# Performance work log

Measured on AMD Instinct MI355X. Metric: run time of the kernel, lower is better.

The kernel has to match this reference:

```python
import jax, jax.numpy as jnp
import numpy as np

K = 1024
D = 512
DECAY = 0.99


def setup_inputs() -> dict:
    key = jax.random.key(0)
    k1, k2, k3 = jax.random.split(key, 3)
    z_e_x = jax.random.normal(k1, (64, 256, D), dtype=jnp.float32)
    codebook = jax.random.normal(k2, (K, D), dtype=jnp.float32)
    ema_count = jnp.ones((K,), dtype=jnp.float32)
    ema_w = jax.random.normal(k3, (K, D), dtype=jnp.float32)
    return {"z_e_x": z_e_x, "codebook": codebook,
            "ema_count": ema_count, "ema_w": ema_w}


def reference(z_e_x, codebook, ema_count, ema_w):
    # --- vector quantization: nearest codebook entry (squared L2) ---
    flat = z_e_x.reshape(-1, D)                       # [N, D]
    cb_sqr = jnp.sum(codebook ** 2, axis=1)           # [K]
    in_sqr = jnp.sum(flat ** 2, axis=1, keepdims=True)  # [N, 1]
    distances = (cb_sqr[None, :] + in_sqr) - 2.0 * (flat @ codebook.T)  # [N, K]
    indices = jnp.argmin(distances, axis=1)           # [N] int

    # straight-through codes from current codebook
    z_q_x = codebook[indices].reshape(z_e_x.shape)

    # --- EMA codebook update (training branch) ---
    counts = jnp.zeros((K,), dtype=flat.dtype).at[indices].add(1.0)       # sum of one-hots
    new_ema_count = DECAY * ema_count + (1.0 - DECAY) * counts
    dw = jnp.zeros((K, D), dtype=flat.dtype).at[indices].add(flat)        # one_hot.T @ flat
    new_ema_w = DECAY * ema_w + (1.0 - DECAY) * dw
    new_embedding = new_ema_w / new_ema_count[:, None]

    # codes from the updated codebook
    z_q_x_bar = new_embedding[indices].reshape(z_e_x.shape)

    return (z_q_x, z_q_x_bar, new_embedding, new_ema_count, new_ema_w)
```

## Files before the change

### kernel.cpp

```cpp
#include <hip/hip_runtime.h>

typedef _Float16 half8  __attribute__((ext_vector_type(8)));
typedef float    f32x4  __attribute__((ext_vector_type(4)));

constexpr int K_CODES = 1024;
constexpr int D_DIM   = 512;
constexpr float DECAY = 0.99f;
constexpr float OMD   = 0.01f;
constexpr float LO_SCALE = 2048.0f;
constexpr float INV_LO   = 1.0f / 2048.0f;

constexpr int BM = 128;
constexpr int BN = 128;
constexpr int BK = 32;
constexpr int NPART = K_CODES / BN;
constexpr int CHUNK = 32;

__global__ __launch_bounds__(256) void zero_kernel(float4* __restrict__ p, int n4) {
    int i = blockIdx.x * 256 + threadIdx.x;
    if (i < n4) p[i] = make_float4(0.f, 0.f, 0.f, 0.f);
}

__global__ __launch_bounds__(64)
void prep_kernel(const float* __restrict__ cb, float* __restrict__ cbsqr,
                 float* __restrict__ counts,
                 _Float16* __restrict__ bh, _Float16* __restrict__ bl) {
    int k = blockIdx.x;
    int lane = threadIdx.x;
    size_t base = (size_t)k * D_DIM + lane * 8;
    f32x4 v0 = *reinterpret_cast<const f32x4*>(&cb[base]);
    f32x4 v1 = *reinterpret_cast<const f32x4*>(&cb[base + 4]);
    half8 h, l;
    float s = 0.f;
    #pragma unroll
    for (int j = 0; j < 4; ++j) {
        s += v0[j] * v0[j];
        _Float16 hh = (_Float16)v0[j];
        h[j] = hh;
        l[j] = (_Float16)((v0[j] - (float)hh) * LO_SCALE);
    }
    #pragma unroll
    for (int j = 0; j < 4; ++j) {
        s += v1[j] * v1[j];
        _Float16 hh = (_Float16)v1[j];
        h[4 + j] = hh;
        l[4 + j] = (_Float16)((v1[j] - (float)hh) * LO_SCALE);
    }
    *reinterpret_cast<half8*>(&bh[base]) = h;
    *reinterpret_cast<half8*>(&bl[base]) = l;
    #pragma unroll
    for (int off = 32; off > 0; off >>= 1) s += __shfl_down(s, off);
    if (lane == 0) { cbsqr[k] = s; counts[k] = 0.f; }
}

__global__ __launch_bounds__(256)
void splitA_kernel(const float* __restrict__ A,
                   _Float16* __restrict__ ah, _Float16* __restrict__ al) {
    size_t i8 = ((size_t)blockIdx.x * 256 + threadIdx.x) * 8;
    f32x4 v0 = *reinterpret_cast<const f32x4*>(&A[i8]);
    f32x4 v1 = *reinterpret_cast<const f32x4*>(&A[i8 + 4]);
    half8 h, l;
    #pragma unroll
    for (int j = 0; j < 4; ++j) {
        _Float16 hh = (_Float16)v0[j];
        h[j] = hh;
        l[j] = (_Float16)((v0[j] - (float)hh) * LO_SCALE);
    }
    #pragma unroll
    for (int j = 0; j < 4; ++j) {
        _Float16 hh = (_Float16)v1[j];
        h[4 + j] = hh;
        l[4 + j] = (_Float16)((v1[j] - (float)hh) * LO_SCALE);
    }
    *reinterpret_cast<half8*>(&ah[i8]) = h;
    *reinterpret_cast<half8*>(&al[i8]) = l;
}

__global__ __launch_bounds__(256, 2)
void argmin_mfma(const _Float16* __restrict__ Ah,
                 const _Float16* __restrict__ Al,
                 const _Float16* __restrict__ Bh,
                 const _Float16* __restrict__ Bl,
                 const float* __restrict__ cbsqr,
                 float* __restrict__ pval,
                 int*   __restrict__ pidx) {
    __shared__ _Float16 Ahs[BM * BK];
    __shared__ _Float16 Als[BM * BK];
    __shared__ _Float16 Bhs[BN * BK];
    __shared__ _Float16 Bls[BN * BK];
    __shared__ float    sv[2][BM];
    __shared__ int      si[2][BM];

    const int tid  = threadIdx.x;
    const int lane = tid & 63;
    const int wid  = tid >> 6;
    const int wr = wid >> 1, wc = wid & 1;
    const int lq = lane >> 4;
    const int lr = lane & 15;

    const int row0  = blockIdx.x * BM;
    const int cbase = blockIdx.y * BN;

    f32x4 acc_h[4][4], acc_c[4][4];
    #pragma unroll
    for (int m = 0; m < 4; ++m)
        #pragma unroll
        for (int n = 0; n < 4; ++n) {
            acc_h[m][n] = f32x4{0.f, 0.f, 0.f, 0.f};
            acc_c[m][n] = f32x4{0.f, 0.f, 0.f, 0.f};
        }

    for (int d0 = 0; d0 < D_DIM; d0 += BK) {
        #pragma unroll
        for (int it = 0; it < 2; ++it) {
            int p = it * 4096 + wid * 1024 + lane * 16;
            int row  = p >> 6;
            int cpos = (p >> 4) & 3;
            int sc   = cpos ^ ((row ^ (row >> 2)) & 3);
            size_t aoff = (size_t)(row0 + row) * D_DIM + d0 + sc * 8;
            size_t boff = (size_t)(cbase + row) * D_DIM + d0 + sc * 8;
            int dst = it * 2048 + wid * 512;
            __builtin_amdgcn_global_load_lds(
                (const __attribute__((address_space(1))) void*)(Ah + aoff),
                (__attribute__((address_space(3))) void*)(Ahs + dst), 16, 0, 0);
            __builtin_amdgcn_global_load_lds(
                (const __attribute__((address_space(1))) void*)(Al + aoff),
                (__attribute__((address_space(3))) void*)(Als + dst), 16, 0, 0);
            __builtin_amdgcn_global_load_lds(
                (const __attribute__((address_space(1))) void*)(Bh + boff),
                (__attribute__((address_space(3))) void*)(Bhs + dst), 16, 0, 0);
            __builtin_amdgcn_global_load_lds(
                (const __attribute__((address_space(1))) void*)(Bl + boff),
                (__attribute__((address_space(3))) void*)(Bls + dst), 16, 0, 0);
        }
        __syncthreads();

        half8 bh[4], bl[4];
        #pragma unroll
        for (int n = 0; n < 4; ++n) {
            int rB  = wc * 64 + n * 16 + lr;
            int pos = lq ^ ((rB ^ (rB >> 2)) & 3);
            bh[n] = *reinterpret_cast<const half8*>(&Bhs[rB * 32 + pos * 8]);
            bl[n] = *reinterpret_cast<const half8*>(&Bls[rB * 32 + pos * 8]);
        }
        #pragma unroll
        for (int m = 0; m < 4; ++m) {
            int rA  = wr * 64 + m * 16 + lr;
            int pos = lq ^ ((rA ^ (rA >> 2)) & 3);
            half8 ah = *reinterpret_cast<const half8*>(&Ahs[rA * 32 + pos * 8]);
            half8 al = *reinterpret_cast<const half8*>(&Als[rA * 32 + pos * 8]);
            #pragma unroll
            for (int n = 0; n < 4; ++n) {
                acc_h[m][n] = __builtin_amdgcn_mfma_f32_16x16x32_f16(ah, bh[n], acc_h[m][n], 0, 0, 0);
                acc_c[m][n] = __builtin_amdgcn_mfma_f32_16x16x32_f16(ah, bl[n], acc_c[m][n], 0, 0, 0);
                acc_c[m][n] = __builtin_amdgcn_mfma_f32_16x16x32_f16(al, bh[n], acc_c[m][n], 0, 0, 0);
            }
        }
        __syncthreads();
    }

    float cs[4];
    #pragma unroll
    for (int n = 0; n < 4; ++n) cs[n] = cbsqr[cbase + wc * 64 + n * 16 + lr];

    #pragma unroll
    for (int m = 0; m < 4; ++m) {
        #pragma unroll
        for (int q = 0; q < 4; ++q) {
            float bv = 3.4e38f;
            int   bi = 0;
            #pragma unroll
            for (int n = 0; n < 4; ++n) {
                float d = cs[n] - 2.0f * acc_h[m][n][q] - (2.0f * INV_LO) * acc_c[m][n][q];
                int   c = cbase + wc * 64 + n * 16 + lr;
                if (d < bv) { bv = d; bi = c; }
            }
            #pragma unroll
            for (int off = 1; off < 16; off <<= 1) {
                float v2 = __shfl_xor(bv, off);
                int   i2 = __shfl_xor(bi, off);
                if (v2 < bv || (v2 == bv && i2 < bi)) { bv = v2; bi = i2; }
            }
            if (lr == 0) {
                int prow = wr * 64 + m * 16 + lq * 4 + q;
                sv[wc][prow] = bv;
                si[wc][prow] = bi;
            }
        }
    }
    __syncthreads();
    if (tid < BM) {
        float v0 = sv[0][tid], v1 = sv[1][tid];
        int   i0 = si[0][tid], i1 = si[1][tid];
        float bv = (v1 < v0) ? v1 : v0;
        int   bi = (v1 < v0) ? i1 : i0;
        pval[(size_t)(row0 + tid) * NPART + blockIdx.y] = bv;
        pidx[(size_t)(row0 + tid) * NPART + blockIdx.y] = bi;
    }
}

__global__ __launch_bounds__(256)
void combine_kernel(const float* __restrict__ pval, const int* __restrict__ pidx,
                    int* __restrict__ indices, float* __restrict__ counts, int N) {
    int r = blockIdx.x * 256 + threadIdx.x;
    if (r >= N) return;
    float bv = pval[(size_t)r * NPART];
    int   bi = pidx[(size_t)r * NPART];
    #pragma unroll
    for (int p = 1; p < NPART; ++p) {
        float v = pval[(size_t)r * NPART + p];
        int  ii = pidx[(size_t)r * NPART + p];
        if (v < bv) { bv = v; bi = ii; }
    }
    indices[r] = bi;
    atomicAdd(&counts[bi], 1.0f);
}

__global__ __launch_bounds__(256)
void scan_kernel(const float* __restrict__ counts,
                 int* __restrict__ offs, int* __restrict__ cursor) {
    __shared__ int part[256];
    int t = threadIdx.x;
    int c[4], s = 0;
    #pragma unroll
    for (int j = 0; j < 4; ++j) { c[j] = (int)counts[t * 4 + j]; s += c[j]; }
    part[t] = s;
    __syncthreads();
    for (int off = 1; off < 256; off <<= 1) {
        int v   = part[t];
        int add = (t >= off) ? part[t - off] : 0;
        __syncthreads();
        part[t] = v + add;
        __syncthreads();
    }
    int run = part[t] - s;
    #pragma unroll
    for (int j = 0; j < 4; ++j) {
        offs[t * 4 + j]   = run;
        cursor[t * 4 + j] = run;
        run += c[j];
    }
    if (t == 255) offs[K_CODES] = part[255];
}

__global__ __launch_bounds__(256)
void scatter_kernel(const int* __restrict__ indices, int* __restrict__ cursor,
                    int* __restrict__ packed, int N) {
    int r = blockIdx.x * 256 + threadIdx.x;
    if (r >= N) return;
    int k = indices[r];
    int pos = atomicAdd(&cursor[k], 1);
    packed[pos] = (k << 16) | r;
}

__global__ __launch_bounds__(128)
void chunksum_kernel(const float* __restrict__ flat, const int* __restrict__ packed,
                     float* __restrict__ dw, int N) {
    __shared__ int ent[CHUNK + 1];
    const int t = threadIdx.x;
    const int base = blockIdx.x * CHUNK;
    const int cnt = min(CHUNK, N - base);
    if (t < cnt) ent[t] = packed[base + t];
    if (t == cnt) ent[t] = -1;
    __syncthreads();

    f32x4 acc = {0.f, 0.f, 0.f, 0.f};
    for (int i0 = 0; i0 < cnt; i0 += 8) {
        const int m = min(8, cnt - i0);
        f32x4 v[8];
        #pragma unroll
        for (int j = 0; j < 8; ++j) {
            if (j < m) {
                int r = ent[i0 + j] & 0xFFFF;
                v[j] = *reinterpret_cast<const f32x4*>(&flat[(size_t)r * D_DIM + t * 4]);
            }
        }
        #pragma unroll
        for (int j = 0; j < 8; ++j) {
            if (j < m) {
                acc[0] += v[j][0]; acc[1] += v[j][1];
                acc[2] += v[j][2]; acc[3] += v[j][3];
                int k = ent[i0 + j] >> 16;
                if ((ent[i0 + j + 1] >> 16) != k) {
                    float* p = &dw[(size_t)k * D_DIM + t * 4];
                    atomicAdd(p + 0, acc[0]);
                    atomicAdd(p + 1, acc[1]);
                    atomicAdd(p + 2, acc[2]);
                    atomicAdd(p + 3, acc[3]);
                    acc = f32x4{0.f, 0.f, 0.f, 0.f};
                }
            }
        }
    }
}

__global__ __launch_bounds__(256)
void finalize_kernel(const float* __restrict__ ema_count, const float* __restrict__ ema_w,
                     const float* __restrict__ counts, const float* __restrict__ dw,
                     float* __restrict__ new_emb, float* __restrict__ new_count,
                     float* __restrict__ new_ema_w) {
    int gid = blockIdx.x * 256 + threadIdx.x;
    int k = gid >> 7;
    int d = (gid & 127) * 4;
    float nc = DECAY * ema_count[k] + OMD * counts[k];
    size_t off = (size_t)k * D_DIM + d;
    float4 w  = *reinterpret_cast<const float4*>(&ema_w[off]);
    float4 dv = *reinterpret_cast<const float4*>(&dw[off]);
    float4 nw;
    nw.x = DECAY * w.x + OMD * dv.x;
    nw.y = DECAY * w.y + OMD * dv.y;
    nw.z = DECAY * w.z + OMD * dv.z;
    nw.w = DECAY * w.w + OMD * dv.w;
    *reinterpret_cast<float4*>(&new_ema_w[off]) = nw;
    float inv = 1.0f / nc;
    float4 ne;
    ne.x = nw.x * inv; ne.y = nw.y * inv; ne.z = nw.z * inv; ne.w = nw.w * inv;
    *reinterpret_cast<float4*>(&new_emb[off]) = ne;
    if ((gid & 127) == 0) new_count[k] = nc;
}

__global__ __launch_bounds__(256)
void gather_kernel(const float* __restrict__ codebook, const float* __restrict__ new_emb,
                   const int* __restrict__ indices,
                   float* __restrict__ zq, float* __restrict__ zqb) {
    int gid = blockIdx.x * 256 + threadIdx.x;
    int r = gid >> 7;
    int d = (gid & 127) * 4;
    int k = indices[r];
    size_t src = (size_t)k * D_DIM + d;
    size_t dst = (size_t)r * D_DIM + d;
    *reinterpret_cast<float4*>(&zq[dst])  = *reinterpret_cast<const float4*>(&codebook[src]);
    *reinterpret_cast<float4*>(&zqb[dst]) = *reinterpret_cast<const float4*>(&new_emb[src]);
}

extern "C" void kernel_launch(void* const* d_in, const int* in_sizes, int n_in,
                              void* d_out, int out_size, void* d_ws, size_t ws_size,
                              hipStream_t stream) {
    const float* z_e_x     = (const float*)d_in[0];
    const float* codebook  = (const float*)d_in[1];
    const float* ema_count = (const float*)d_in[2];
    const float* ema_w     = (const float*)d_in[3];

    const int N = in_sizes[0] / D_DIM;

    float* out = (float*)d_out;
    float* z_q_x     = out;
    float* z_q_x_bar = z_q_x + (size_t)N * D_DIM;
    float* new_emb   = z_q_x_bar + (size_t)N * D_DIM;
    float* new_count = new_emb + (size_t)K_CODES * D_DIM;
    float* new_ema_w = new_count + K_CODES;

    _Float16* Ahs = (_Float16*)z_q_x_bar;
    _Float16* Als = Ahs + (size_t)N * D_DIM;

    char* ws = (char*)d_ws;
    int*   indices = (int*)ws;
    float* cbsqr   = (float*)(ws + (size_t)N * 4);
    float* pval    = cbsqr + K_CODES;
    int*   pidx    = (int*)(pval + (size_t)N * NPART);
    float* counts  = (float*)(pidx + (size_t)N * NPART);
    _Float16* bh   = (_Float16*)(counts + K_CODES);
    _Float16* bl   = bh + (size_t)K_CODES * D_DIM;
    float* dw      = (float*)bh;
    int*   offs    = (int*)(bl + (size_t)K_CODES * D_DIM);
    int*   cursor  = offs + K_CODES + 1;
    int*   packed  = cursor + K_CODES;

    prep_kernel<<<K_CODES, 64, 0, stream>>>(codebook, cbsqr, counts, bh, bl);
    splitA_kernel<<<(N * D_DIM / 8) / 256, 256, 0, stream>>>(z_e_x, Ahs, Als);

    dim3 g_argmin(N / BM, K_CODES / BN);
    argmin_mfma<<<g_argmin, 256, 0, stream>>>(Ahs, Als, bh, bl, cbsqr, pval, pidx);

    combine_kernel<<<(N + 255) / 256, 256, 0, stream>>>(pval, pidx, indices, counts, N);

    scan_kernel<<<1, 256, 0, stream>>>(counts, offs, cursor);
    scatter_kernel<<<(N + 255) / 256, 256, 0, stream>>>(indices, cursor, packed, N);

    zero_kernel<<<(K_CODES * D_DIM / 4) / 256, 256, 0, stream>>>((float4*)dw, K_CODES * D_DIM / 4);
    chunksum_kernel<<<(N + CHUNK - 1) / CHUNK, 128, 0, stream>>>(z_e_x, packed, dw, N);

    finalize_kernel<<<(K_CODES * (D_DIM / 4)) / 256, 256, 0, stream>>>(
        ema_count, ema_w, counts, dw, new_emb, new_count, new_ema_w);

    gather_kernel<<<(N * (D_DIM / 4)) / 256, 256, 0, stream>>>(
        codebook, new_emb, indices, z_q_x, z_q_x_bar);
}
```

Before: 143.6 us.

## Double-buffer argmin LDS tiles and merge small launch kernels

The argmin GEMM loop now double-buffers its LDS tiles: the next K-slice is issued with async global-to-LDS loads before the current slice's MFMAs run, leaving one barrier per step instead of two. Separately, the codebook prep and input split kernels are merged into one launch, and the dw zeroing is merged with the scatter kernel, removing two launches. Double buffering doubles LDS use per block, which may cut occupancy below the two blocks per CU the launch bounds request.

```diff
diff --git a/kernel.cpp b/kernel.cpp
--- a/kernel.cpp
+++ b/kernel.cpp
@@ -13,67 +13,65 @@
 constexpr int BM = 128;
 constexpr int BN = 128;
 constexpr int BK = 32;
+constexpr int TILE = BM * BK;
 constexpr int NPART = K_CODES / BN;
 constexpr int CHUNK = 32;
 
-__global__ __launch_bounds__(256) void zero_kernel(float4* __restrict__ p, int n4) {
-    int i = blockIdx.x * 256 + threadIdx.x;
-    if (i < n4) p[i] = make_float4(0.f, 0.f, 0.f, 0.f);
-}
-
-__global__ __launch_bounds__(64)
-void prep_kernel(const float* __restrict__ cb, float* __restrict__ cbsqr,
-                 float* __restrict__ counts,
-                 _Float16* __restrict__ bh, _Float16* __restrict__ bl) {
-    int k = blockIdx.x;
-    int lane = threadIdx.x;
-    size_t base = (size_t)k * D_DIM + lane * 8;
-    f32x4 v0 = *reinterpret_cast<const f32x4*>(&cb[base]);
-    f32x4 v1 = *reinterpret_cast<const f32x4*>(&cb[base + 4]);
-    half8 h, l;
-    float s = 0.f;
-    #pragma unroll
-    for (int j = 0; j < 4; ++j) {
-        s += v0[j] * v0[j];
-        _Float16 hh = (_Float16)v0[j];
-        h[j] = hh;
-        l[j] = (_Float16)((v0[j] - (float)hh) * LO_SCALE);
-    }
-    #pragma unroll
-    for (int j = 0; j < 4; ++j) {
-        s += v1[j] * v1[j];
-        _Float16 hh = (_Float16)v1[j];
-        h[4 + j] = hh;
-        l[4 + j] = (_Float16)((v1[j] - (float)hh) * LO_SCALE);
-    }
-    *reinterpret_cast<half8*>(&bh[base]) = h;
-    *reinterpret_cast<half8*>(&bl[base]) = l;
-    #pragma unroll
-    for (int off = 32; off > 0; off >>= 1) s += __shfl_down(s, off);
-    if (lane == 0) { cbsqr[k] = s; counts[k] = 0.f; }
-}
-
-__global__ __launch_bounds__(256)
-void splitA_kernel(const float* __restrict__ A,
-                   _Float16* __restrict__ ah, _Float16* __restrict__ al) {
-    size_t i8 = ((size_t)blockIdx.x * 256 + threadIdx.x) * 8;
-    f32x4 v0 = *reinterpret_cast<const f32x4*>(&A[i8]);
-    f32x4 v1 = *reinterpret_cast<const f32x4*>(&A[i8 + 4]);
-    half8 h, l;
-    #pragma unroll
-    for (int j = 0; j < 4; ++j) {
-        _Float16 hh = (_Float16)v0[j];
-        h[j] = hh;
-        l[j] = (_Float16)((v0[j] - (float)hh) * LO_SCALE);
-    }
-    #pragma unroll
-    for (int j = 0; j < 4; ++j) {
-        _Float16 hh = (_Float16)v1[j];
-        h[4 + j] = hh;
-        l[4 + j] = (_Float16)((v1[j] - (float)hh) * LO_SCALE);
-    }
-    *reinterpret_cast<half8*>(&ah[i8]) = h;
-    *reinterpret_cast<half8*>(&al[i8]) = l;
+__global__ __launch_bounds__(256)
+void prepsplit_kernel(const float* __restrict__ A, const float* __restrict__ cb,
+                      float* __restrict__ cbsqr, float* __restrict__ counts,
+                      _Float16* __restrict__ ah, _Float16* __restrict__ al,
+                      _Float16* __restrict__ bh, _Float16* __restrict__ bl,
+                      int nA) {
+    int b = blockIdx.x;
+    if (b < nA) {
+        size_t i8 = ((size_t)b * 256 + threadIdx.x) * 8;
+        f32x4 v0 = *reinterpret_cast<const f32x4*>(&A[i8]);
+        f32x4 v1 = *reinterpret_cast<const f32x4*>(&A[i8 + 4]);
+        half8 h, l;
+        #pragma unroll
+        for (int j = 0; j < 4; ++j) {
+            _Float16 hh = (_Float16)v0[j];
+            h[j] = hh;
+            l[j] = (_Float16)((v0[j] - (float)hh) * LO_SCALE);
+        }
+        #pragma unroll
+        for (int j = 0; j < 4; ++j) {
+            _Float16 hh = (_Float16)v1[j];
+            h[4 + j] = hh;
+            l[4 + j] = (_Float16)((v1[j] - (float)hh) * LO_SCALE);
+        }
+        *reinterpret_cast<half8*>(&ah[i8]) = h;
+        *reinterpret_cast<half8*>(&al[i8]) = l;
+    } else {
+        int w    = threadIdx.x >> 6;
+        int lane = threadIdx.x & 63;
+        int k = (b - nA) * 4 + w;
+        size_t base = (size_t)k * D_DIM + lane * 8;
+        f32x4 v0 = *reinterpret_cast<const f32x4*>(&cb[base]);
+        f32x4 v1 = *reinterpret_cast<const f32x4*>(&cb[base + 4]);
+        half8 h, l;
+        float s = 0.f;
+        #pragma unroll
+        for (int j = 0; j < 4; ++j) {
+            s += v0[j] * v0[j];
+            _Float16 hh = (_Float16)v0[j];
+            h[j] = hh;
+            l[j] = (_Float16)((v0[j] - (float)hh) * LO_SCALE);
+        }
+        #pragma unroll
+        for (int j = 0; j < 4; ++j) {
+            s += v1[j] * v1[j];
+            _Float16 hh = (_Float16)v1[j];
+            h[4 + j] = hh;
+            l[4 + j] = (_Float16)((v1[j] - (float)hh) * LO_SCALE);
+        }
+        *reinterpret_cast<half8*>(&bh[base]) = h;
+        *reinterpret_cast<half8*>(&bl[base]) = l;
+        #pragma unroll
+        for (int off = 32; off > 0; off >>= 1) s += __shfl_down(s, off);
+        if (lane == 0) { cbsqr[k] = s; counts[k] = 0.f; }
+    }
 }
 
 __global__ __launch_bounds__(256, 2)
@@ -84,10 +82,10 @@
                  const float* __restrict__ cbsqr,
                  float* __restrict__ pval,
                  int*   __restrict__ pidx) {
-    __shared__ _Float16 Ahs[BM * BK];
-    __shared__ _Float16 Als[BM * BK];
-    __shared__ _Float16 Bhs[BN * BK];
-    __shared__ _Float16 Bls[BN * BK];
+    __shared__ _Float16 Ahs[2][TILE];
+    __shared__ _Float16 Als[2][TILE];
+    __shared__ _Float16 Bhs[2][TILE];
+    __shared__ _Float16 Bls[2][TILE];
     __shared__ float    sv[2][BM];
     __shared__ int      si[2][BM];
 
@@ -110,7 +108,7 @@
             acc_c[m][n] = f32x4{0.f, 0.f, 0.f, 0.f};
         }
 
-    for (int d0 = 0; d0 < D_DIM; d0 += BK) {
+    auto stage = [&](int buf, int d0) {
         #pragma unroll
         for (int it = 0; it < 2; ++it) {
             int p = it * 4096 + wid * 1024 + lane * 16;
@@ -122,33 +120,41 @@
             int dst = it * 2048 + wid * 512;
             __builtin_amdgcn_global_load_lds(
                 (const __attribute__((address_space(1))) void*)(Ah + aoff),
-                (__attribute__((address_space(3))) void*)(Ahs + dst), 16, 0, 0);
+                (__attribute__((address_space(3))) void*)(&Ahs[buf][dst]), 16, 0, 0);
             __builtin_amdgcn_global_load_lds(
                 (const __attribute__((address_space(1))) void*)(Al + aoff),
-                (__attribute__((address_space(3))) void*)(Als + dst), 16, 0, 0);
+                (__attribute__((address_space(3))) void*)(&Als[buf][dst]), 16, 0, 0);
             __builtin_amdgcn_global_load_lds(
                 (const __attribute__((address_space(1))) void*)(Bh + boff),
-                (__attribute__((address_space(3))) void*)(Bhs + dst), 16, 0, 0);
+                (__attribute__((address_space(3))) void*)(&Bhs[buf][dst]), 16, 0, 0);
             __builtin_amdgcn_global_load_lds(
                 (const __attribute__((address_space(1))) void*)(Bl + boff),
-                (__attribute__((address_space(3))) void*)(Bls + dst), 16, 0, 0);
-        }
-        __syncthreads();
+                (__attribute__((address_space(3))) void*)(&Bls[buf][dst]), 16, 0, 0);
+        }
+    };
+
+    stage(0, 0);
+    __syncthreads();
+
+    constexpr int NSTEP = D_DIM / BK;
+    for (int t = 0; t < NSTEP; ++t) {
+        const int buf = t & 1;
+        if (t + 1 < NSTEP) stage(buf ^ 1, (t + 1) * BK);
 
         half8 bh[4], bl[4];
         #pragma unroll
         for (int n = 0; n < 4; ++n) {
             int rB  = wc * 64 + n * 16 + lr;
             int pos = lq ^ ((rB ^ (rB >> 2)) & 3);
-            bh[n] = *reinterpret_cast<const half8*>(&Bhs[rB * 32 + pos * 8]);
-            bl[n] = *reinterpret_cast<const half8*>(&Bls[rB * 32 + pos * 8]);
+            bh[n] = *reinterpret_cast<const half8*>(&Bhs[buf][rB * 32 + pos * 8]);
+            bl[n] = *reinterpret_cast<const half8*>(&Bls[buf][rB * 32 + pos * 8]);
         }
         #pragma unroll
         for (int m = 0; m < 4; ++m) {
             int rA  = wr * 64 + m * 16 + lr;
             int pos = lq ^ ((rA ^ (rA >> 2)) & 3);
-            half8 ah = *reinterpret_cast<const half8*>(&Ahs[rA * 32 + pos * 8]);
-            half8 al = *reinterpret_cast<const half8*>(&Als[rA * 32 + pos * 8]);
+            half8 ah = *reinterpret_cast<const half8*>(&Ahs[buf][rA * 32 + pos * 8]);
+            half8 al = *reinterpret_cast<const half8*>(&Als[buf][rA * 32 + pos * 8]);
             #pragma unroll
             for (int n = 0; n < 4; ++n) {
                 acc_h[m][n] = __builtin_amdgcn_mfma_f32_16x16x32_f16(ah, bh[n], acc_h[m][n], 0, 0, 0);
@@ -244,13 +250,19 @@
 }
 
 __global__ __launch_bounds__(256)
-void scatter_kernel(const int* __restrict__ indices, int* __restrict__ cursor,
-                    int* __restrict__ packed, int N) {
-    int r = blockIdx.x * 256 + threadIdx.x;
-    if (r >= N) return;
-    int k = indices[r];
-    int pos = atomicAdd(&cursor[k], 1);
-    packed[pos] = (k << 16) | r;
+void zeroscatter_kernel(const int* __restrict__ indices, int* __restrict__ cursor,
+                        int* __restrict__ packed, float4* __restrict__ dw,
+                        int N, int nzero) {
+    int b = blockIdx.x;
+    if (b < nzero) {
+        dw[b * 256 + threadIdx.x] = make_float4(0.f, 0.f, 0.f, 0.f);
+    } else {
+        int r = (b - nzero) * 256 + threadIdx.x;
+        if (r >= N) return;
+        int k = indices[r];
+        int pos = atomicAdd(&cursor[k], 1);
+        packed[pos] = (k << 16) | r;
+    }
 }
 
 __global__ __launch_bounds__(128)
@@ -350,8 +362,8 @@
     float* new_count = new_emb + (size_t)K_CODES * D_DIM;
     float* new_ema_w = new_count + K_CODES;
 
-    _Float16* Ahs = (_Float16*)z_q_x_bar;
-    _Float16* Als = Ahs + (size_t)N * D_DIM;
+    _Float16* Ahp = (_Float16*)z_q_x_bar;
+    _Float16* Alp = Ahp + (size_t)N * D_DIM;
 
     char* ws = (char*)d_ws;
     int*   indices = (int*)ws;
@@ -366,18 +378,21 @@
     int*   cursor  = offs + K_CODES + 1;
     int*   packed  = cursor + K_CODES;
 
-    prep_kernel<<<K_CODES, 64, 0, stream>>>(codebook, cbsqr, counts, bh, bl);
-    splitA_kernel<<<(N * D_DIM / 8) / 256, 256, 0, stream>>>(z_e_x, Ahs, Als);
+    const int nA = (N * D_DIM / 8) / 256;
+    prepsplit_kernel<<<nA + K_CODES / 4, 256, 0, stream>>>(
+        z_e_x, codebook, cbsqr, counts, Ahp, Alp, bh, bl, nA);
 
     dim3 g_argmin(N / BM, K_CODES / BN);
-    argmin_mfma<<<g_argmin, 256, 0, stream>>>(Ahs, Als, bh, bl, cbsqr, pval, pidx);
+    argmin_mfma<<<g_argmin, 256, 0, stream>>>(Ahp, Alp, bh, bl, cbsqr, pval, pidx);
 
     combine_kernel<<<(N + 255) / 256, 256, 0, stream>>>(pval, pidx, indices, counts, N);
 
     scan_kernel<<<1, 256, 0, stream>>>(counts, offs, cursor);
-    scatter_kernel<<<(N + 255) / 256, 256, 0, stream>>>(indices, cursor, packed, N);
-
-    zero_kernel<<<(K_CODES * D_DIM / 4) / 256, 256, 0, stream>>>((float4*)dw, K_CODES * D_DIM / 4);
+
+    const int nzero = (K_CODES * D_DIM / 4) / 256;
+    zeroscatter_kernel<<<nzero + (N + 255) / 256, 256, 0, stream>>>(
+        indices, cursor, packed, (float4*)dw, N, nzero);
+
     chunksum_kernel<<<(N + CHUNK - 1) / CHUNK, 128, 0, stream>>>(z_e_x, packed, dw, N);
 
     finalize_kernel<<<(K_CODES * (D_DIM / 4)) / 256, 256, 0, stream>>>(
```

New measurement: 140.7 us. -2.1%, faster.
